# Kernel optimization log

Measured on AMD Instinct MI355X. Metric: run time of the kernel, lower is better.

## Reference

```python
import jax, jax.numpy as jnp
import numpy as np

B, T, H, N = 1, 256, 32, 128
HN = H * N
KVH = 8
KV_DIM = KVH * N
KV_REPEAT = HN // KV_DIM
ROPE_THETA = 10000.0
EPS = 1e-6
NTK_ALPHA = 10.0
YARN_MAX = 4096.0
LORA_W, LORA_A, LORA_V, LORA_G = 64, 64, 32, 128
LAYER_ID = 1


def t5_rmsnorm(x, w):
    xf = x.astype(jnp.float32)
    var = jnp.mean(xf * xf, axis=-1, keepdims=True)
    return (w * (xf * jax.lax.rsqrt(var + EPS))).astype(x.dtype)


def rotate_half(x):
    h = x.shape[-1] // 2
    return jnp.concatenate([-x[..., h:], x[..., :h]], axis=-1)


def rope_cache(cache_pos, seq_len, rotary_dim):
    # YaRN-style mix of short/long inv_freq, per compute_rope_cache_range
    half = rotary_dim // 2
    fs = jnp.arange(half, dtype=jnp.float32)
    inv_short = 1.0 / ROPE_THETA ** (fs / half)
    inv_long = 1.0 / (ROPE_THETA * NTK_ALPHA ** (fs / half))
    pos = cache_pos.astype(jnp.float32) + jnp.arange(seq_len, dtype=jnp.float32)[None, :]  # [B,T]
    mix = jnp.clip(pos / YARN_MAX, 0.0, 1.0)[..., None]
    freqs = (1.0 - mix) * (pos[..., None] * inv_short) + mix * (pos[..., None] * inv_long)
    emb = jnp.concatenate([freqs, freqs], axis=-1)  # [B,T,rotary_dim]
    return jnp.cos(emb), jnp.sin(emb)


def _forward(x_in, v_first, state, cache_position, w0, w1, w2, a0, a1, a2, v0, v1, v2, g1, g2,
             r_k, R_, K_, V_, O_, R_bias, K_bias, V_bias, ln_r, ln_k, ln1, ln2):
    x = t5_rmsnorm(x_in, ln1)  # [B,T,HN]
    # float path of fpx_matmul: x @ W.T (+ bias), i.e. the dequantized math
    r = x @ R_.T + R_bias
    k = x @ K_.T + K_bias
    v = x @ V_.T + V_bias
    r = t5_rmsnorm(r.reshape(B, T, H, N), ln_r)      # [B,T,H,N]
    k = t5_rmsnorm(k.reshape(B, T, KVH, N), ln_k)    # [B,T,KVH,N]
    cos, sin = rope_cache(cache_position, T, N)      # [B,T,N]
    cos_, sin_ = cos[:, :, None, :], sin[:, :, None, :]
    r = r * cos_ + rotate_half(r) * sin_
    k = k * cos_ + rotate_half(k) * sin_
    # decay lora: w = -softplus(-(tanh(x@w1)@w2 + w0)) - 0.5
    w = jnp.tanh(x @ w1) @ w2 + w0
    w = -jax.nn.softplus(-w) - 0.5
    # GQA repeat_kv: each kv head repeated KV_REPEAT times contiguously
    v = v.reshape(B, T, KVH, N)
    k = jnp.repeat(k, KV_REPEAT, axis=2).reshape(B, T, HN)
    v = jnp.repeat(v, KV_REPEAT, axis=2).reshape(B, T, HN)
    a = jax.nn.sigmoid((x @ a1) @ a2 + a0)
    g = jax.nn.sigmoid(x @ g1) @ g2
    k4 = k.reshape(B, T, H, N)
    kk = (k4 / jnp.maximum(jnp.linalg.norm(k4, axis=-1, keepdims=True), 1e-12)).reshape(B, T, HN)
    k = k * (1.0 - w + a)
    aa = -kk
    bb = kk * a
    if LAYER_ID == 0:
        v_first = v
    else:
        gate = jax.nn.sigmoid((x @ v1) @ v2 + v0)
        v = v + (v_first - v) * gate
    w = -jnp.exp(w.astype(jnp.float32))  # log-decay for the recurrence

    def to_tm(t):  # [B,T,HN] or [B,T,H,N] -> time-major [T,B,H,N]
        return jnp.moveaxis(t.reshape(B, T, H, N), 1, 0)

    rt, wt, kt, vt, at, bt = map(to_tm, (r, w, k, v, aa, bb))

    def step(S, inp):
        # RWKV-7: S = S*diag(exp(w)) + S @ (a b^T) + v k^T ; out = S @ r
        r_t, w_t, k_t, v_t, a_t, b_t = inp
        sa = jnp.einsum('bhij,bhj->bhi', S, a_t)
        S = S * jnp.exp(w_t)[:, :, None, :] + sa[..., None] * b_t[:, :, None, :] + v_t[..., None] * k_t[:, :, None, :]
        return S, jnp.einsum('bhij,bhj->bhi', S, r_t)

    S_final, outs = jax.lax.scan(step, state.astype(jnp.float32), (rt, wt, kt, vt, at, bt))
    xx = jnp.moveaxis(outs, 0, 1).reshape(B, T, HN) * (float(N) ** -0.5)
    bonus = jnp.sum(r.reshape(B, T, H, N) * k.reshape(B, T, H, N) * r_k, axis=-1, keepdims=True) * v.reshape(B, T, H, N)
    xx = xx.astype(r.dtype) + bonus.reshape(B, T, HN)
    x_res = x_in + (xx * g) @ O_.T
    out = t5_rmsnorm(x_res, ln2)
    return out, x[:, -1], S_final, v_first, x_res


def setup_inputs() -> dict:
    key = jax.random.key(0)
    ks = iter(jax.random.split(key, 32))
    rn = lambda *s: jax.random.normal(next(ks), s, dtype=jnp.float32)
    wt = lambda *s: rn(*s) * 0.02
    return dict(
        x_in=rn(B, T, HN),
        v_first=rn(B, T, HN),
        state=jnp.zeros((B, H, N, N), jnp.float32),
        cache_position=jnp.zeros((B, 1), jnp.int32),
        w0=wt(HN), w1=wt(HN, LORA_W), w2=wt(LORA_W, HN),
        a0=wt(HN), a1=wt(HN, LORA_A), a2=wt(LORA_A, HN),
        v0=wt(HN), v1=wt(HN, LORA_V), v2=wt(LORA_V, HN),
        g1=wt(HN, LORA_G), g2=wt(LORA_G, HN),
        r_k=wt(H, N),
        R_=wt(HN, HN), K_=wt(KV_DIM, HN), V_=wt(KV_DIM, HN), O_=wt(HN, HN),
        R_bias=wt(HN), K_bias=wt(KV_DIM), V_bias=wt(KV_DIM),
        ln_r=jnp.ones((N,), jnp.float32), ln_k=jnp.ones((N,), jnp.float32),
        ln1=jnp.ones((HN,), jnp.float32), ln2=jnp.ones((HN,), jnp.float32),
    )


def reference(x_in, v_first, state, cache_position, w0, w1, w2, a0, a1, a2, v0, v1, v2, g1, g2,
              r_k, R_, K_, V_, O_, R_bias, K_bias, V_bias, ln_r, ln_k, ln1, ln2):
    return _forward(x_in, v_first, state, cache_position, w0, w1, w2, a0, a1, a2, v0, v1, v2,
                    g1, g2, r_k, R_, K_, V_, O_, R_bias, K_bias, V_bias, ln_r, ln_k, ln1, ln2)
```

## Files before the change

### kernel.cpp

```cpp
#include <hip/hip_runtime.h>
#include <cstdint>
#include <cstddef>

#define T_ 256
#define HN_ 4096
#define H_ 32
#define N_ 128
#define SR_ 6464

typedef __attribute__((ext_vector_type(8))) short short8;
typedef __attribute__((ext_vector_type(4))) float f32x4;

__device__ __forceinline__ short f2bf(float f) {
    uint32_t u = __builtin_bit_cast(uint32_t, f);
    u = (u + 0x7fffu + ((u >> 16) & 1u)) >> 16;
    return (short)u;
}
__device__ __forceinline__ short f2bfc(float f) {
    return (short)((__builtin_bit_cast(uint32_t, f) + 0x8000u) >> 16);
}
__device__ __forceinline__ short8 cvt8r(float4 lo, float4 hi) {
    short8 v;
    v[0] = f2bfc(lo.x); v[1] = f2bfc(lo.y); v[2] = f2bfc(lo.z); v[3] = f2bfc(lo.w);
    v[4] = f2bfc(hi.x); v[5] = f2bfc(hi.y); v[6] = f2bfc(hi.z); v[7] = f2bfc(hi.w);
    return v;
}
__device__ __forceinline__ f32x4 mfma16(short8 a, short8 b, f32x4 c) {
    return __builtin_amdgcn_mfma_f32_16x16x32_bf16(a, b, c, 0, 0, 0);
}
__device__ __forceinline__ float sigm(float x) { return 1.f / (1.f + expf(-x)); }
__device__ __forceinline__ float splus(float x) { return (x > 20.f) ? x : log1pf(expf(x)); }

__device__ __forceinline__ float bf1(ushort u) {
    return __builtin_bit_cast(float, (uint32_t)u << 16);
}
__device__ __forceinline__ void bf4(float* d, const ushort* p) {
    uint2 u = *(const uint2*)p;
    d[0] = __builtin_bit_cast(float, u.x << 16);
    d[1] = __builtin_bit_cast(float, u.x & 0xffff0000u);
    d[2] = __builtin_bit_cast(float, u.y << 16);
    d[3] = __builtin_bit_cast(float, u.y & 0xffff0000u);
}
__device__ __forceinline__ void gload_lds16(const void* g, void* l) {
    __builtin_amdgcn_global_load_lds(
        (const __attribute__((address_space(1))) void*)g,
        (__attribute__((address_space(3))) void*)l, 16, 0, 0);
}

template <int CTRL>
__device__ __forceinline__ float dpp_add(float v) {
    int p = __builtin_amdgcn_mov_dpp(__builtin_bit_cast(int, v), CTRL, 0xF, 0xF, true);
    return v + __builtin_bit_cast(float, p);
}
__device__ __forceinline__ float reduce32(float v) {
    v = dpp_add<0xB1>(v);
    v = dpp_add<0x4E>(v);
    v = dpp_add<0x124>(v);
    v = dpp_add<0x128>(v);
    v += __shfl_xor(v, 16);
    return v;
}

__device__ __forceinline__ void gemm_core(
    const ushort* __restrict__ A, const float* __restrict__ Brow,
    int kbeg, float* LB, f32x4 acc[2][2]) {
    const int tid = threadIdx.x, wid = tid >> 6, l = tid & 63;
    const int ar = l & 15, ak = (l >> 4) * 8;
    const int mBase = wid * 32;

    const int p1 = tid, p2 = tid + 512;
    const int r1 = p1 >> 5, c1 = (p1 & 31) ^ (r1 & 7);
    const int r2 = p2 >> 5, c2 = (p2 & 31) ^ (r2 & 7);
    const float* sb1 = Brow + (size_t)r1 * 4096 + kbeg + c1 * 4;
    const float* sb2 = Brow + (size_t)r2 * 4096 + kbeg + c2 * 4;
    float* d1 = LB + wid * 256;
    float* d2 = LB + 2048 + wid * 256;

    const ushort* pa0 = A + (size_t)(mBase + ar) * 4096 + kbeg + ak;
    const ushort* pa1 = pa0 + (size_t)16 * 4096;

    const int rb0 = ar * 128, rb1 = (16 + ar) * 128;
    const int sx = ar & 7;
    const int cb = (l >> 4) * 2;

    short8 Ae[8], Ao[8];

#define STAGEB(s, rb) { \
    gload_lds16(sb1 + (size_t)(s) * 128, d1 + (rb) * 4096); \
    gload_lds16(sb2 + (size_t)(s) * 128, d2 + (rb) * 4096); }

#define LA(B_, s) { \
    B_[0] = *(const short8*)(pa0 + (size_t)(s) * 128);      \
    B_[1] = *(const short8*)(pa1 + (size_t)(s) * 128);      \
    B_[2] = *(const short8*)(pa0 + (size_t)(s) * 128 + 32); \
    B_[3] = *(const short8*)(pa1 + (size_t)(s) * 128 + 32); \
    B_[4] = *(const short8*)(pa0 + (size_t)(s) * 128 + 64); \
    B_[5] = *(const short8*)(pa1 + (size_t)(s) * 128 + 64); \
    B_[6] = *(const short8*)(pa0 + (size_t)(s) * 128 + 96); \
    B_[7] = *(const short8*)(pa1 + (size_t)(s) * 128 + 96); }

#define CKK(kk, B_, Lb_) { \
    const int cc = (kk) * 8 + cb; \
    float4 l0 = *(const float4*)(Lb_ + rb0 + ((cc ^ sx) * 4)); \
    float4 h0 = *(const float4*)(Lb_ + rb0 + (((cc + 1) ^ sx) * 4)); \
    float4 l1 = *(const float4*)(Lb_ + rb1 + ((cc ^ sx) * 4)); \
    float4 h1 = *(const float4*)(Lb_ + rb1 + (((cc + 1) ^ sx) * 4)); \
    short8 b0 = cvt8r(l0, h0), b1 = cvt8r(l1, h1); \
    acc[0][0] = mfma16(B_[2 * (kk)], b0, acc[0][0]); \
    acc[0][1] = mfma16(B_[2 * (kk)], b1, acc[0][1]); \
    acc[1][0] = mfma16(B_[2 * (kk) + 1], b0, acc[1][0]); \
    acc[1][1] = mfma16(B_[2 * (kk) + 1], b1, acc[1][1]); }

#define COMPUTE(rb, B_) { const float* Lb_ = LB + (rb) * 4096; \
    CKK(0, B_, Lb_) CKK(1, B_, Lb_) CKK(2, B_, Lb_) CKK(3, B_, Lb_) }

    STAGEB(0, 0)
    LA(Ae, 0)
    STAGEB(1, 1)

    for (int su = 0; su < 4; su++) {
        const int s0 = su * 2, s1 = su * 2 + 1;
        LA(Ao, (s0 + 1 < 8) ? s0 + 1 : 7)
        STAGEB((s0 + 2 < 8) ? s0 + 2 : 7, (s0 + 2) % 3)
        asm volatile("s_waitcnt vmcnt(12)" ::: "memory");
        __builtin_amdgcn_s_barrier();
        __builtin_amdgcn_sched_barrier(0);
        COMPUTE(s0 % 3, Ae)
        __builtin_amdgcn_s_barrier();

        LA(Ae, (s1 + 1 < 8) ? s1 + 1 : 7)
        STAGEB((s1 + 2 < 8) ? s1 + 2 : 7, (s1 + 2) % 3)
        asm volatile("s_waitcnt vmcnt(12)" ::: "memory");
        __builtin_amdgcn_s_barrier();
        __builtin_amdgcn_sched_barrier(0);
        COMPUTE(s1 % 3, Ao)
        __builtin_amdgcn_s_barrier();
    }
    asm volatile("s_waitcnt vmcnt(0)" ::: "memory");
#undef STAGEB
#undef LA
#undef CKK
#undef COMPUTE
}

__global__ __launch_bounds__(256) void rmsnorm_k(const float* __restrict__ in,
                                                 const float* __restrict__ w,
                                                 float* __restrict__ outF,
                                                 ushort* __restrict__ outB,
                                                 float* __restrict__ lastrow) {
    int t = blockIdx.x, tid = threadIdx.x;
    const float4* in4 = (const float4*)(in + (size_t)t * HN_);
    const float4* w4 = (const float4*)w;
    float4 v[4]; float ss = 0.f;
#pragma unroll
    for (int q = 0; q < 4; q++) {
        v[q] = in4[q * 256 + tid];
        ss += v[q].x * v[q].x + v[q].y * v[q].y + v[q].z * v[q].z + v[q].w * v[q].w;
    }
#pragma unroll
    for (int o = 32; o; o >>= 1) ss += __shfl_down(ss, o);
    __shared__ float red[4];
    if ((tid & 63) == 0) red[tid >> 6] = ss;
    __syncthreads();
    float tot = red[0] + red[1] + red[2] + red[3];
    float sc = rsqrtf(tot * (1.f / HN_) + 1e-6f);
#pragma unroll
    for (int q = 0; q < 4; q++) {
        float4 wv = w4[q * 256 + tid];
        float4 r;
        r.x = wv.x * v[q].x * sc; r.y = wv.y * v[q].y * sc;
        r.z = wv.z * v[q].z * sc; r.w = wv.w * v[q].w * sc;
        int idx = q * 256 + tid;
        if (outF) ((float4*)(outF + (size_t)t * HN_))[idx] = r;
        if (outB) {
            ushort4 b;
            b.x = (ushort)f2bf(r.x); b.y = (ushort)f2bf(r.y);
            b.z = (ushort)f2bf(r.z); b.w = (ushort)f2bf(r.w);
            ((ushort4*)(outB + (size_t)t * HN_))[idx] = b;
        }
        if (lastrow && t == T_ - 1) ((float4*)lastrow)[idx] = r;
    }
}

__global__ __launch_bounds__(512, 2) void gemm_rkvt(
    const ushort* __restrict__ A,
    const float* __restrict__ Rw, const float* __restrict__ Kw,
    const float* __restrict__ Vw, const float* __restrict__ WT,
    float* __restrict__ COMB) {
    __shared__ __align__(16) float LB[12288];
    const int tid = threadIdx.x, wid = tid >> 6, l = tid & 63;
    const int mBase = wid * 32;
    const int nB = blockIdx.x * 32;
    const int kbeg = blockIdx.y * 1024;

    const float* Bp; int brow;
    if (nB < 4096)      { Bp = Rw; brow = nB; }
    else if (nB < 5120) { Bp = Kw; brow = nB - 4096; }
    else if (nB < 6144) { Bp = Vw; brow = nB - 5120; }
    else                { Bp = WT; brow = nB - 6144; }

    f32x4 acc[2][2];
#pragma unroll
    for (int i = 0; i < 2; i++)
#pragma unroll
        for (int j = 0; j < 2; j++) acc[i][j] = f32x4{0.f, 0.f, 0.f, 0.f};

    gemm_core(A, Bp + (size_t)brow * 4096, kbeg, LB, acc);

    const int rl = (l >> 4) * 4, cl = l & 15;
#pragma unroll
    for (int mf = 0; mf < 2; mf++)
#pragma unroll
        for (int nf = 0; nf < 2; nf++)
#pragma unroll
            for (int e = 0; e < 4; e++)
                unsafeAtomicAdd(&COMB[(size_t)(mBase + mf * 16 + rl + e) * SR_ + nB + nf * 16 + cl],
                                acc[mf][nf][e]);
}

__global__ __launch_bounds__(512, 2) void gemm_o(
    const ushort* __restrict__ A,
    const float* __restrict__ B,
    float* __restrict__ C) {
    __shared__ __align__(16) float LB[12288];
    const int tid = threadIdx.x, wid = tid >> 6, l = tid & 63;
    const int mBase = wid * 32;
    const int nB = blockIdx.x * 32;
    const int kbeg = blockIdx.y * 1024;

    f32x4 acc[2][2];
#pragma unroll
    for (int i = 0; i < 2; i++)
#pragma unroll
        for (int j = 0; j < 2; j++) acc[i][j] = f32x4{0.f, 0.f, 0.f, 0.f};

    gemm_core(A, B + (size_t)nB * 4096, kbeg, LB, acc);

    const int rl = (l >> 4) * 4, cl = l & 15;
#pragma unroll
    for (int mf = 0; mf < 2; mf++)
#pragma unroll
        for (int nf = 0; nf < 2; nf++)
#pragma unroll
            for (int e = 0; e < 4; e++)
                unsafeAtomicAdd(&C[(size_t)(mBase + mf * 16 + rl + e) * 4096 + nB + nf * 16 + cl],
                                acc[mf][nf][e]);
}

__global__ __launch_bounds__(512) void gemm_s2(
    const ushort* __restrict__ TCB,
    const float* __restrict__ w2, const float* __restrict__ a2,
    const float* __restrict__ v2, const float* __restrict__ g2,
    const float* __restrict__ w0, const float* __restrict__ a0,
    const float* __restrict__ v0,
    float* __restrict__ WPRE, float* __restrict__ APRE,
    float* __restrict__ VGPRE, float* __restrict__ GARR) {
    const int z = blockIdx.y;
    int Aoff, K; const float* B; const float* bias; float* out;
    if (z == 0)      { Aoff = 0;   K = 64;  B = w2; bias = w0;      out = WPRE; }
    else if (z == 1) { Aoff = 64;  K = 64;  B = a2; bias = a0;      out = APRE; }
    else if (z == 2) { Aoff = 128; K = 32;  B = v2; bias = v0;      out = VGPRE; }
    else             { Aoff = 160; K = 128; B = g2; bias = nullptr; out = GARR; }

    const int tid = threadIdx.x, wid = tid >> 6, l = tid & 63;
    const int ar = l & 15, ak = (l >> 4) * 8;
    const int mBase = wid * 32;
    const int nB = blockIdx.x * 32;

    f32x4 acc[2][2];
#pragma unroll
    for (int i = 0; i < 2; i++)
#pragma unroll
        for (int j = 0; j < 2; j++) acc[i][j] = f32x4{0.f, 0.f, 0.f, 0.f};

    for (int k0 = 0; k0 < K; k0 += 32) {
        const ushort* pA = TCB + (size_t)(mBase + ar) * 320 + Aoff + k0 + ak;
        short8 av0 = *(const short8*)pA;
        short8 av1 = *(const short8*)(pA + (size_t)16 * 320);
        short8 bv0, bv1;
#pragma unroll
        for (int e = 0; e < 8; e++) {
            bv0[e] = f2bfc(B[(size_t)(k0 + ak + e) * 4096 + nB + ar]);
            bv1[e] = f2bfc(B[(size_t)(k0 + ak + e) * 4096 + nB + 16 + ar]);
        }
        acc[0][0] = mfma16(av0, bv0, acc[0][0]);
        acc[0][1] = mfma16(av0, bv1, acc[0][1]);
        acc[1][0] = mfma16(av1, bv0, acc[1][0]);
        acc[1][1] = mfma16(av1, bv1, acc[1][1]);
    }
    const int rl = (l >> 4) * 4, cl = l & 15;
#pragma unroll
    for (int mf = 0; mf < 2; mf++)
#pragma unroll
        for (int nf = 0; nf < 2; nf++) {
            int col = nB + nf * 16 + cl;
            float bv = bias ? bias[col] : 0.f;
#pragma unroll
            for (int e = 0; e < 4; e++)
                out[(size_t)(mBase + mf * 16 + rl + e) * 4096 + col] = acc[mf][nf][e] + bv;
        }
}

__global__ __launch_bounds__(256) void wcat2_k(const float* __restrict__ w1p,
                                               const float* __restrict__ a1p,
                                               const float* __restrict__ v1p,
                                               const float* __restrict__ g1p,
                                               float* __restrict__ WT) {
    const int kb = blockIdx.x * 64, tile = blockIdx.y;
    const float* src; int ldw, jo, nb, W;
    if (tile == 0)      { src = w1p; ldw = 64;  jo = 0;  nb = 0;   W = 64; }
    else if (tile == 1) { src = a1p; ldw = 64;  jo = 0;  nb = 64;  W = 64; }
    else if (tile == 2) { src = v1p; ldw = 32;  jo = 0;  nb = 128; W = 32; }
    else if (tile == 3) { src = g1p; ldw = 128; jo = 0;  nb = 160; W = 64; }
    else                { src = g1p; ldw = 128; jo = 64; nb = 224; W = 64; }
    __shared__ float lds[64][65];
    const int ti = threadIdx.x & 63, wi = threadIdx.x >> 6;
    if (ti < W)
        for (int i = wi; i < 64; i += 4)
            lds[i][ti] = src[(size_t)(kb + i) * ldw + jo + ti];
    __syncthreads();
    for (int i2 = wi; i2 < W; i2 += 4)
        WT[(size_t)(nb + i2) * 4096 + kb + ti] = lds[ti][i2];
}

__global__ __launch_bounds__(256) void init_comb_k(const float* __restrict__ Rb,
                                                   const float* __restrict__ Kb,
                                                   const float* __restrict__ Vb,
                                                   float* __restrict__ COMB) {
    int t = blockIdx.x;
    for (int c = threadIdx.x; c < SR_; c += 256) {
        float b = (c < 4096) ? Rb[c] : (c < 5120) ? Kb[c - 4096]
                : (c < 6144) ? Vb[c - 5120] : 0.f;
        COMB[(size_t)t * SR_ + c] = b;
    }
}

__global__ __launch_bounds__(256) void act_k(const float* __restrict__ COMB,
                                             ushort* __restrict__ TCB) {
    int idx = blockIdx.x * 256 + threadIdx.x;
    if (idx >= 256 * 288) return;
    int t = idx / 288, c = idx % 288;
    float v = COMB[(size_t)t * SR_ + 6144 + c];
    if (c < 64) v = tanhf(v);
    else if (c >= 160) v = sigm(v);
    TCB[t * 320 + c] = (ushort)f2bf(v);
}

__global__ void rope_k(const int* __restrict__ cpos, float* __restrict__ cosT,
                       float* __restrict__ sinT) {
    int idx = blockIdx.x * 256 + threadIdx.x;
    int t = idx >> 6, f = idx & 63;
    float pos = (float)cpos[0] + (float)t;
    float mix = fminf(fmaxf(pos * (1.f / 4096.f), 0.f), 1.f);
    float e = (float)f * (1.f / 64.f);
    float inv_s = exp2f(-13.287712379549449f * e);
    float inv_l = exp2f(-13.287712379549449f - 3.321928094887362f * e);
    float fr = pos * ((1.f - mix) * inv_s + mix * inv_l);
    cosT[idx] = cosf(fr);
    sinT[idx] = sinf(fr);
}

__global__ __launch_bounds__(256) void prep_k(
    const float* __restrict__ COMB, const float* __restrict__ wpre,
    const float* __restrict__ apre, const float* __restrict__ vgpre,
    const float* __restrict__ vfirst, const float* __restrict__ garr,
    const float* __restrict__ cosT, const float* __restrict__ sinT,
    const float* __restrict__ lnr, const float* __restrict__ lnk,
    ushort* __restrict__ SFB) {
    int t = blockIdx.x, tid = threadIdx.x;
    int w = tid >> 6, lane = tid & 63;
    float c = cosT[t * 64 + lane], s = sinT[t * 64 + lane];
    float lr0 = lnr[lane], lr1 = lnr[lane + 64];
    float lk0 = lnk[lane], lk1 = lnk[lane + 64];
    const float* r_raw = COMB;
    const float* k_raw = COMB + 4096;
    const float* v_raw = COMB + 5120;
    for (int hb = 0; hb < 8; hb++) {
        int h = hb * 4 + w;
        int kv = h >> 2;
        float r0 = r_raw[(size_t)t * SR_ + h * 128 + lane];
        float r1 = r_raw[(size_t)t * SR_ + h * 128 + 64 + lane];
        float ssum = r0 * r0 + r1 * r1;
#pragma unroll
        for (int o = 32; o; o >>= 1) ssum += __shfl_xor(ssum, o);
        float sc = rsqrtf(ssum * (1.f / 128.f) + 1e-6f);
        float rn0 = lr0 * r0 * sc, rn1 = lr1 * r1 * sc;
        float rr0 = rn0 * c - rn1 * s;
        float rr1 = rn1 * c + rn0 * s;
        float k0 = k_raw[(size_t)t * SR_ + kv * 128 + lane];
        float k1 = k_raw[(size_t)t * SR_ + kv * 128 + 64 + lane];
        float ks = k0 * k0 + k1 * k1;
#pragma unroll
        for (int o = 32; o; o >>= 1) ks += __shfl_xor(ks, o);
        float ksc = rsqrtf(ks * (1.f / 128.f) + 1e-6f);
        float kn0 = lk0 * k0 * ksc, kn1 = lk1 * k1 * ksc;
        float kr0 = kn0 * c - kn1 * s;
        float kr1 = kn1 * c + kn0 * s;
        float nr = kr0 * kr0 + kr1 * kr1;
#pragma unroll
        for (int o = 32; o; o >>= 1) nr += __shfl_xor(nr, o);
        float inv = 1.f / fmaxf(sqrtf(nr), 1e-12f);
        float kk0 = kr0 * inv, kk1 = kr1 * inv;
        int c0 = h * 128 + lane, c1 = c0 + 64;
        size_t tb = (size_t)t * HN_;

        float wv0 = -splus(-wpre[tb + c0]) - 0.5f;
        float wv1 = -splus(-wpre[tb + c1]) - 0.5f;
        float dec0 = expf(-expf(wv0));
        float dec1 = expf(-expf(wv1));
        float av0 = sigm(apre[tb + c0]);
        float av1 = sigm(apre[tb + c1]);
        float vg0 = sigm(vgpre[tb + c0]);
        float vg1 = sigm(vgpre[tb + c1]);
        float vraw0 = v_raw[(size_t)t * SR_ + kv * 128 + lane];
        float vraw1 = v_raw[(size_t)t * SR_ + kv * 128 + 64 + lane];
        float vf0 = vraw0 + (vfirst[tb + c0] - vraw0) * vg0;
        float vf1 = vraw1 + (vfirst[tb + c1] - vraw1) * vg1;

        ushort* sb = SFB + ((size_t)h * T_ + t) * 1024;
        sb[lane]         = (ushort)f2bf(rr0);
        sb[64 + lane]    = (ushort)f2bf(rr1);
        sb[128 + lane]   = (ushort)f2bf(kr0 * (1.f - wv0 + av0));
        sb[192 + lane]   = (ushort)f2bf(kr1 * (1.f - wv1 + av1));
        sb[256 + lane]   = (ushort)f2bf(vf0);
        sb[320 + lane]   = (ushort)f2bf(vf1);
        sb[384 + lane]   = (ushort)f2bf(-kk0);
        sb[448 + lane]   = (ushort)f2bf(-kk1);
        sb[512 + lane]   = (ushort)f2bf(kk0 * av0);
        sb[576 + lane]   = (ushort)f2bf(kk1 * av1);
        sb[640 + lane]   = (ushort)f2bf(garr[tb + c0]);
        sb[704 + lane]   = (ushort)f2bf(garr[tb + c1]);
        float* sw = (float*)(sb + 768);
        sw[lane]      = dec0;
        sw[64 + lane] = dec1;
    }
}

#define SD_ 8
#define SNB_ 9
__global__ __launch_bounds__(512) void scan_k(
    const float* __restrict__ state_in,
    const ushort* __restrict__ SFB,
    const float* __restrict__ rk,
    ushort* __restrict__ yb, float* __restrict__ Sout) {
    const int h = blockIdx.x, sp = blockIdx.y;
    const int tid = threadIdx.x;
    const int il = tid >> 5, jq = tid & 31;
    const int i = sp * 16 + il, j0 = jq * 4;
    const int wv = tid >> 6;

    float S[4];
    {
        float4 s4 = *(const float4*)(state_in + ((size_t)h * 128 + i) * 128 + j0);
        S[0] = s4.x; S[1] = s4.y; S[2] = s4.z; S[3] = s4.w;
    }
    float4 rk4 = *(const float4*)(rk + h * 128 + j0);

    __shared__ __align__(16) ushort lds_s[SNB_][1024];
    __shared__ float ybuf[2][16];
    const ushort* hbase = SFB + (size_t)h * T_ * 1024;

    auto STAGE = [&](int buf, int t) {
        if (tid < 128) {
            const ushort* src = hbase + (size_t)(t & (T_ - 1)) * 1024 + tid * 8;
            gload_lds16(src, &lds_s[buf][wv * 512]);
        }
    };

#pragma unroll
    for (int d = 0; d < SD_; d++) STAGE(d, d);

    float cpPend = 0.f;
    int bc = 0, bs = SD_;
    for (int t = 0; t < T_; t++) {
        if (wv < 2) asm volatile("s_waitcnt vmcnt(7)" ::: "memory");
        __builtin_amdgcn_s_barrier();
        __builtin_amdgcn_sched_barrier(0);
        asm volatile("" ::: "memory");

        STAGE(bs, t + SD_);

        if (wv == 7 && (tid & 63) < 16 && t > 1) {
            int ln = tid & 63;
            yb[(size_t)(t - 2) * HN_ + h * 128 + sp * 16 + ln] =
                (ushort)f2bf(ybuf[t & 1][ln]);
        }

        if (t > 0) {
            float cr = reduce32(cpPend);
            if (jq == 0) ybuf[(t - 1) & 1][il] = cr;
        }

        const ushort* L = lds_s[bc];
        float r_[4], k_[4], a_[4], b_[4];
        bf4(r_, L + j0);
        bf4(k_, L + 128 + j0);
        bf4(a_, L + 384 + j0);
        bf4(b_, L + 512 + j0);
        float vi = bf1(L[256 + i]);
        float gv = bf1(L[640 + i]);
        const float* Ld = (const float*)(L + 768);
        float4 w4 = *(const float4*)&Ld[j0];

        float sa = fmaf(S[0], a_[0], fmaf(S[1], a_[1], fmaf(S[2], a_[2], S[3] * a_[3])));
        sa = reduce32(sa);

        S[0] = fmaf(vi, k_[0], fmaf(sa, b_[0], S[0] * w4.x));
        S[1] = fmaf(vi, k_[1], fmaf(sa, b_[1], S[1] * w4.y));
        S[2] = fmaf(vi, k_[2], fmaf(sa, b_[2], S[2] * w4.z));
        S[3] = fmaf(vi, k_[3], fmaf(sa, b_[3], S[3] * w4.w));

        float od = fmaf(S[0], r_[0], fmaf(S[1], r_[1], fmaf(S[2], r_[2], S[3] * r_[3])));
        float bd = fmaf(r_[0] * k_[0], rk4.x, fmaf(r_[1] * k_[1], rk4.y,
                   fmaf(r_[2] * k_[2], rk4.z, r_[3] * k_[3] * rk4.w)));
        cpPend = fmaf(od, 0.08838834764831845f, bd * vi) * gv;

        bc = (bc + 1 == SNB_) ? 0 : bc + 1;
        bs = (bs + 1 == SNB_) ? 0 : bs + 1;
    }

    __builtin_amdgcn_s_barrier();
    {
        float cr = reduce32(cpPend);
        if (jq == 0)
            yb[(size_t)(T_ - 1) * HN_ + h * 128 + i] = (ushort)f2bf(cr);
    }
    if (wv == 7 && (tid & 63) < 16) {
        int ln = tid & 63;
        yb[(size_t)(T_ - 2) * HN_ + h * 128 + sp * 16 + ln] =
            (ushort)f2bf(ybuf[(T_ - 2) & 1][ln]);
    }

    float* p = Sout + ((size_t)h * 128 + i) * 128 + j0;
    *(float4*)p = make_float4(S[0], S[1], S[2], S[3]);
}

extern "C" void kernel_launch(void* const* d_in, const int* in_sizes, int n_in,
                              void* d_out, int out_size, void* d_ws, size_t ws_size,
                              hipStream_t stream) {
    const float* x_in   = (const float*)d_in[0];
    const float* vfirst = (const float*)d_in[1];
    const float* state  = (const float*)d_in[2];
    const int*   cpos   = (const int*)d_in[3];
    const float* w0 = (const float*)d_in[4];
    const float* w1 = (const float*)d_in[5];
    const float* w2 = (const float*)d_in[6];
    const float* a0 = (const float*)d_in[7];
    const float* a1 = (const float*)d_in[8];
    const float* a2 = (const float*)d_in[9];
    const float* v0 = (const float*)d_in[10];
    const float* v1 = (const float*)d_in[11];
    const float* v2 = (const float*)d_in[12];
    const float* g1 = (const float*)d_in[13];
    const float* g2 = (const float*)d_in[14];
    const float* r_k = (const float*)d_in[15];
    const float* R_ = (const float*)d_in[16];
    const float* K_ = (const float*)d_in[17];
    const float* V_ = (const float*)d_in[18];
    const float* O_ = (const float*)d_in[19];
    const float* Rb = (const float*)d_in[20];
    const float* Kb = (const float*)d_in[21];
    const float* Vb = (const float*)d_in[22];
    const float* ln_r = (const float*)d_in[23];
    const float* ln_k = (const float*)d_in[24];
    const float* ln1 = (const float*)d_in[25];
    const float* ln2 = (const float*)d_in[26];

    float* ws = (float*)d_ws;
    constexpr size_t OFF_XB   = 0;
    constexpr size_t OFF_COMB = 524288;
    constexpr size_t OFF_WT   = 2179072;
    constexpr size_t OFF_TCB  = 3489792;
    constexpr size_t OFF_WPRE = 3530752;
    constexpr size_t OFF_APRE = 4579328;
    constexpr size_t OFF_VGPRE= 5627904;
    constexpr size_t OFF_G    = 6676480;
    constexpr size_t OFF_COS  = 7725056;
    constexpr size_t OFF_SIN  = 7741440;
    constexpr size_t OFF_SF   = 7757824;
    constexpr size_t OFF_YB   = OFF_XB;

    ushort* XB  = (ushort*)(ws + OFF_XB);
    float* COMB = ws + OFF_COMB;
    float* WT   = ws + OFF_WT;
    ushort* TCB = (ushort*)(ws + OFF_TCB);
    float* WPRE = ws + OFF_WPRE;
    float* APRE = ws + OFF_APRE;
    float* VGPRE= ws + OFF_VGPRE;
    float* GARR = ws + OFF_G;
    float* COST = ws + OFF_COS;
    float* SINT = ws + OFF_SIN;
    ushort* SFB = (ushort*)(ws + OFF_SF);
    ushort* YB  = (ushort*)(ws + OFF_YB);

    float* out = (float*)d_out;
    float* out0  = out;
    float* xlast = out + 1048576;
    float* Sfin  = out + 1052672;
    float* vfout = out + 1576960;
    float* xres  = out + 2625536;

    hipMemcpyAsync(vfout, vfirst, (size_t)1048576 * 4, hipMemcpyDeviceToDevice, stream);
    hipMemcpyAsync(xres, x_in, (size_t)1048576 * 4, hipMemcpyDeviceToDevice, stream);

    rmsnorm_k<<<T_, 256, 0, stream>>>(x_in, ln1, nullptr, XB, xlast);

    wcat2_k<<<dim3(64, 5), 256, 0, stream>>>(w1, a1, v1, g1, WT);
    hipMemsetAsync(WT + (size_t)288 * 4096, 0, (size_t)32 * 4096 * 4, stream);
    init_comb_k<<<T_, 256, 0, stream>>>(Rb, Kb, Vb, COMB);

    gemm_rkvt<<<dim3(202, 4), 512, 0, stream>>>(XB, R_, K_, V_, WT, COMB);

    act_k<<<288, 256, 0, stream>>>(COMB, TCB);

    gemm_s2<<<dim3(128, 4), 512, 0, stream>>>(TCB, w2, a2, v2, g2, w0, a0, v0,
                                              WPRE, APRE, VGPRE, GARR);

    rope_k<<<64, 256, 0, stream>>>(cpos, COST, SINT);

    prep_k<<<T_, 256, 0, stream>>>(COMB, WPRE, APRE, VGPRE, vfirst, GARR,
                                   COST, SINT, ln_r, ln_k, SFB);

    scan_k<<<dim3(32, 8), 512, 0, stream>>>(state, SFB, r_k, YB, Sfin);

    gemm_o<<<dim3(128, 4), 512, 0, stream>>>(YB, O_, xres);

    rmsnorm_k<<<T_, 256, 0, stream>>>(xres, ln2, out0, nullptr, nullptr);
}
```

Baseline: 329.3 us.

## Process two heads per scan block to interleave independent recurrences

```diff
diff --git a/kernel.cpp b/kernel.cpp
--- a/kernel.cpp
+++ b/kernel.cpp
@@ -443,26 +443,34 @@
     const ushort* __restrict__ SFB,
     const float* __restrict__ rk,
     ushort* __restrict__ yb, float* __restrict__ Sout) {
-    const int h = blockIdx.x, sp = blockIdx.y;
+    const int hp = blockIdx.x, sp = blockIdx.y;
+    const int h0 = hp * 2, h1 = hp * 2 + 1;
     const int tid = threadIdx.x;
     const int il = tid >> 5, jq = tid & 31;
     const int i = sp * 16 + il, j0 = jq * 4;
     const int wv = tid >> 6;
 
-    float S[4];
+    float SA[4], SB[4];
     {
-        float4 s4 = *(const float4*)(state_in + ((size_t)h * 128 + i) * 128 + j0);
-        S[0] = s4.x; S[1] = s4.y; S[2] = s4.z; S[3] = s4.w;
-    }
-    float4 rk4 = *(const float4*)(rk + h * 128 + j0);
-
-    __shared__ __align__(16) ushort lds_s[SNB_][1024];
-    __shared__ float ybuf[2][16];
-    const ushort* hbase = SFB + (size_t)h * T_ * 1024;
+        float4 s4 = *(const float4*)(state_in + ((size_t)h0 * 128 + i) * 128 + j0);
+        SA[0] = s4.x; SA[1] = s4.y; SA[2] = s4.z; SA[3] = s4.w;
+        float4 s5 = *(const float4*)(state_in + ((size_t)h1 * 128 + i) * 128 + j0);
+        SB[0] = s5.x; SB[1] = s5.y; SB[2] = s5.z; SB[3] = s5.w;
+    }
+    float4 rkA = *(const float4*)(rk + h0 * 128 + j0);
+    float4 rkB = *(const float4*)(rk + h1 * 128 + j0);
+
+    __shared__ __align__(16) ushort lds_s[SNB_][2048];
+    __shared__ float ybuf[2][32];
+    const ushort* hb0 = SFB + (size_t)h0 * T_ * 1024;
+    const ushort* hb1 = SFB + (size_t)h1 * T_ * 1024;
 
     auto STAGE = [&](int buf, int t) {
-        if (tid < 128) {
-            const ushort* src = hbase + (size_t)(t & (T_ - 1)) * 1024 + tid * 8;
+        if (tid < 256) {
+            int tw = t & (T_ - 1);
+            const ushort* src = (tid < 128)
+                ? hb0 + (size_t)tw * 1024 + tid * 8
+                : hb1 + (size_t)tw * 1024 + (tid - 128) * 8;
             gload_lds16(src, &lds_s[buf][wv * 512]);
         }
     };
@@ -470,50 +478,67 @@
 #pragma unroll
     for (int d = 0; d < SD_; d++) STAGE(d, d);
 
-    float cpPend = 0.f;
+    float cpA = 0.f, cpB = 0.f;
     int bc = 0, bs = SD_;
     for (int t = 0; t < T_; t++) {
-        if (wv < 2) asm volatile("s_waitcnt vmcnt(7)" ::: "memory");
+        if (wv < 4) asm volatile("s_waitcnt vmcnt(7)" ::: "memory");
         __builtin_amdgcn_s_barrier();
         __builtin_amdgcn_sched_barrier(0);
         asm volatile("" ::: "memory");
 
         STAGE(bs, t + SD_);
 
-        if (wv == 7 && (tid & 63) < 16 && t > 1) {
+        if (wv == 7 && (tid & 63) < 32 && t > 1) {
             int ln = tid & 63;
-            yb[(size_t)(t - 2) * HN_ + h * 128 + sp * 16 + ln] =
+            int hh = (ln < 16) ? h0 : h1;
+            yb[(size_t)(t - 2) * HN_ + hh * 128 + sp * 16 + (ln & 15)] =
                 (ushort)f2bf(ybuf[t & 1][ln]);
         }
 
         if (t > 0) {
-            float cr = reduce32(cpPend);
-            if (jq == 0) ybuf[(t - 1) & 1][il] = cr;
+            float crA = reduce32(cpA);
+            float crB = reduce32(cpB);
+            if (jq == 0) {
+                ybuf[(t - 1) & 1][il] = crA;
+                ybuf[(t - 1) & 1][16 + il] = crB;
+            }
         }
 
-        const ushort* L = lds_s[bc];
-        float r_[4], k_[4], a_[4], b_[4];
-        bf4(r_, L + j0);
-        bf4(k_, L + 128 + j0);
-        bf4(a_, L + 384 + j0);
-        bf4(b_, L + 512 + j0);
-        float vi = bf1(L[256 + i]);
-        float gv = bf1(L[640 + i]);
-        const float* Ld = (const float*)(L + 768);
-        float4 w4 = *(const float4*)&Ld[j0];
-
-        float sa = fmaf(S[0], a_[0], fmaf(S[1], a_[1], fmaf(S[2], a_[2], S[3] * a_[3])));
-        sa = reduce32(sa);
-
-        S[0] = fmaf(vi, k_[0], fmaf(sa, b_[0], S[0] * w4.x));
-        S[1] = fmaf(vi, k_[1], fmaf(sa, b_[1], S[1] * w4.y));
-        S[2] = fmaf(vi, k_[2], fmaf(sa, b_[2], S[2] * w4.z));
-        S[3] = fmaf(vi, k_[3], fmaf(sa, b_[3], S[3] * w4.w));
-
-        float od = fmaf(S[0], r_[0], fmaf(S[1], r_[1], fmaf(S[2], r_[2], S[3] * r_[3])));
-        float bd = fmaf(r_[0] * k_[0], rk4.x, fmaf(r_[1] * k_[1], rk4.y,
-                   fmaf(r_[2] * k_[2], rk4.z, r_[3] * k_[3] * rk4.w)));
-        cpPend = fmaf(od, 0.08838834764831845f, bd * vi) * gv;
+        const ushort* L0 = &lds_s[bc][0];
+        const ushort* L1 = &lds_s[bc][1024];
+        float rA[4], kA[4], aA[4], bA[4];
+        float rB[4], kB[4], aB[4], bB[4];
+        bf4(rA, L0 + j0);        bf4(rB, L1 + j0);
+        bf4(kA, L0 + 128 + j0);  bf4(kB, L1 + 128 + j0);
+        bf4(aA, L0 + 384 + j0);  bf4(aB, L1 + 384 + j0);
+        bf4(bA, L0 + 512 + j0);  bf4(bB, L1 + 512 + j0);
+        float viA = bf1(L0[256 + i]), viB = bf1(L1[256 + i]);
+        float gvA = bf1(L0[640 + i]), gvB = bf1(L1[640 + i]);
+        float4 wA = *(const float4*)((const float*)(L0 + 768) + j0);
+        float4 wB = *(const float4*)((const float*)(L1 + 768) + j0);
+
+        float saA = fmaf(SA[0], aA[0], fmaf(SA[1], aA[1], fmaf(SA[2], aA[2], SA[3] * aA[3])));
+        float saB = fmaf(SB[0], aB[0], fmaf(SB[1], aB[1], fmaf(SB[2], aB[2], SB[3] * aB[3])));
+        saA = reduce32(saA);
+        saB = reduce32(saB);
+
+        SA[0] = fmaf(viA, kA[0], fmaf(saA, bA[0], SA[0] * wA.x));
+        SB[0] = fmaf(viB, kB[0], fmaf(saB, bB[0], SB[0] * wB.x));
+        SA[1] = fmaf(viA, kA[1], fmaf(saA, bA[1], SA[1] * wA.y));
+        SB[1] = fmaf(viB, kB[1], fmaf(saB, bB[1], SB[1] * wB.y));
+        SA[2] = fmaf(viA, kA[2], fmaf(saA, bA[2], SA[2] * wA.z));
+        SB[2] = fmaf(viB, kB[2], fmaf(saB, bB[2], SB[2] * wB.z));
+        SA[3] = fmaf(viA, kA[3], fmaf(saA, bA[3], SA[3] * wA.w));
+        SB[3] = fmaf(viB, kB[3], fmaf(saB, bB[3], SB[3] * wB.w));
+
+        float odA = fmaf(SA[0], rA[0], fmaf(SA[1], rA[1], fmaf(SA[2], rA[2], SA[3] * rA[3])));
+        float odB = fmaf(SB[0], rB[0], fmaf(SB[1], rB[1], fmaf(SB[2], rB[2], SB[3] * rB[3])));
+        float bdA = fmaf(rA[0] * kA[0], rkA.x, fmaf(rA[1] * kA[1], rkA.y,
+                    fmaf(rA[2] * kA[2], rkA.z, rA[3] * kA[3] * rkA.w)));
+        float bdB = fmaf(rB[0] * kB[0], rkB.x, fmaf(rB[1] * kB[1], rkB.y,
+                    fmaf(rB[2] * kB[2], rkB.z, rB[3] * kB[3] * rkB.w)));
+        cpA = fmaf(odA, 0.08838834764831845f, bdA * viA) * gvA;
+        cpB = fmaf(odB, 0.08838834764831845f, bdB * viB) * gvB;
 
         bc = (bc + 1 == SNB_) ? 0 : bc + 1;
         bs = (bs + 1 == SNB_) ? 0 : bs + 1;
@@ -521,18 +546,24 @@
 
     __builtin_amdgcn_s_barrier();
     {
-        float cr = reduce32(cpPend);
-        if (jq == 0)
-            yb[(size_t)(T_ - 1) * HN_ + h * 128 + i] = (ushort)f2bf(cr);
-    }
-    if (wv == 7 && (tid & 63) < 16) {
+        float crA = reduce32(cpA);
+        float crB = reduce32(cpB);
+        if (jq == 0) {
+            yb[(size_t)(T_ - 1) * HN_ + h0 * 128 + i] = (ushort)f2bf(crA);
+            yb[(size_t)(T_ - 1) * HN_ + h1 * 128 + i] = (ushort)f2bf(crB);
+        }
+    }
+    if (wv == 7 && (tid & 63) < 32) {
         int ln = tid & 63;
-        yb[(size_t)(T_ - 2) * HN_ + h * 128 + sp * 16 + ln] =
+        int hh = (ln < 16) ? h0 : h1;
+        yb[(size_t)(T_ - 2) * HN_ + hh * 128 + sp * 16 + (ln & 15)] =
             (ushort)f2bf(ybuf[(T_ - 2) & 1][ln]);
     }
 
-    float* p = Sout + ((size_t)h * 128 + i) * 128 + j0;
-    *(float4*)p = make_float4(S[0], S[1], S[2], S[3]);
+    float* pA = Sout + ((size_t)h0 * 128 + i) * 128 + j0;
+    *(float4*)pA = make_float4(SA[0], SA[1], SA[2], SA[3]);
+    float* pB = Sout + ((size_t)h1 * 128 + i) * 128 + j0;
+    *(float4*)pB = make_float4(SB[0], SB[1], SB[2], SB[3]);
 }
 
 extern "C" void kernel_launch(void* const* d_in, const int* in_sizes, int n_in,
@@ -621,7 +652,7 @@
     prep_k<<<T_, 256, 0, stream>>>(COMB, WPRE, APRE, VGPRE, vfirst, GARR,
                                    COST, SINT, ln_r, ln_k, SFB);
 
-    scan_k<<<dim3(32, 8), 512, 0, stream>>>(state, SFB, r_k, YB, Sfin);
+    scan_k<<<dim3(16, 8), 512, 0, stream>>>(state, SFB, r_k, YB, Sfin);
 
     gemm_o<<<dim3(128, 4), 512, 0, stream>>>(YB, O_, xres);
 
```

New measurement: 395.9 us. +20.2%, slower.

## Split scan state rows across twice as many blocks with 2 columns per lane

Applied to the files above, without the earlier changes.

```diff
diff --git a/kernel.cpp b/kernel.cpp
--- a/kernel.cpp
+++ b/kernel.cpp
@@ -34,13 +34,6 @@
 __device__ __forceinline__ float bf1(ushort u) {
     return __builtin_bit_cast(float, (uint32_t)u << 16);
 }
-__device__ __forceinline__ void bf4(float* d, const ushort* p) {
-    uint2 u = *(const uint2*)p;
-    d[0] = __builtin_bit_cast(float, u.x << 16);
-    d[1] = __builtin_bit_cast(float, u.x & 0xffff0000u);
-    d[2] = __builtin_bit_cast(float, u.y << 16);
-    d[3] = __builtin_bit_cast(float, u.y & 0xffff0000u);
-}
 __device__ __forceinline__ void gload_lds16(const void* g, void* l) {
     __builtin_amdgcn_global_load_lds(
         (const __attribute__((address_space(1))) void*)g,
@@ -52,13 +45,15 @@
     int p = __builtin_amdgcn_mov_dpp(__builtin_bit_cast(int, v), CTRL, 0xF, 0xF, true);
     return v + __builtin_bit_cast(float, p);
 }
-__device__ __forceinline__ float reduce32(float v) {
+__device__ __forceinline__ float reduce64(float v) {
     v = dpp_add<0xB1>(v);
     v = dpp_add<0x4E>(v);
     v = dpp_add<0x124>(v);
     v = dpp_add<0x128>(v);
-    v += __shfl_xor(v, 16);
-    return v;
+    v = dpp_add<0x142>(v);
+    v = dpp_add<0x143>(v);
+    int r = __builtin_amdgcn_readlane(__builtin_bit_cast(int, v), 63);
+    return __builtin_bit_cast(float, r);
 }
 
 __device__ __forceinline__ void gemm_core(
@@ -445,19 +440,19 @@
     ushort* __restrict__ yb, float* __restrict__ Sout) {
     const int h = blockIdx.x, sp = blockIdx.y;
     const int tid = threadIdx.x;
-    const int il = tid >> 5, jq = tid & 31;
-    const int i = sp * 16 + il, j0 = jq * 4;
-    const int wv = tid >> 6;
-
-    float S[4];
+    const int wv = tid >> 6, ln = tid & 63;
+    const int i = sp * 8 + wv;
+    const int j0 = ln * 2;
+
+    float S0, S1;
     {
-        float4 s4 = *(const float4*)(state_in + ((size_t)h * 128 + i) * 128 + j0);
-        S[0] = s4.x; S[1] = s4.y; S[2] = s4.z; S[3] = s4.w;
-    }
-    float4 rk4 = *(const float4*)(rk + h * 128 + j0);
+        float2 s2 = *(const float2*)(state_in + ((size_t)h * 128 + i) * 128 + j0);
+        S0 = s2.x; S1 = s2.y;
+    }
+    float2 rk2 = *(const float2*)(rk + h * 128 + j0);
 
     __shared__ __align__(16) ushort lds_s[SNB_][1024];
-    __shared__ float ybuf[2][16];
+    __shared__ float ybuf[2][8];
     const ushort* hbase = SFB + (size_t)h * T_ * 1024;
 
     auto STAGE = [&](int buf, int t) {
@@ -480,39 +475,37 @@
 
         STAGE(bs, t + SD_);
 
-        if (wv == 7 && (tid & 63) < 16 && t > 1) {
-            int ln = tid & 63;
-            yb[(size_t)(t - 2) * HN_ + h * 128 + sp * 16 + ln] =
+        if (wv == 7 && ln < 8 && t > 1) {
+            yb[(size_t)(t - 2) * HN_ + h * 128 + sp * 8 + ln] =
                 (ushort)f2bf(ybuf[t & 1][ln]);
         }
 
         if (t > 0) {
-            float cr = reduce32(cpPend);
-            if (jq == 0) ybuf[(t - 1) & 1][il] = cr;
+            float cr = reduce64(cpPend);
+            if (ln == 0) ybuf[(t - 1) & 1][wv] = cr;
         }
 
         const ushort* L = lds_s[bc];
-        float r_[4], k_[4], a_[4], b_[4];
-        bf4(r_, L + j0);
-        bf4(k_, L + 128 + j0);
-        bf4(a_, L + 384 + j0);
-        bf4(b_, L + 512 + j0);
+        uint ur = *(const uint*)(L + j0);
+        uint uk = *(const uint*)(L + 128 + j0);
+        uint ua = *(const uint*)(L + 384 + j0);
+        uint ub = *(const uint*)(L + 512 + j0);
+        float r0 = bf1((ushort)ur), r1 = bf1((ushort)(ur >> 16));
+        float k0 = bf1((ushort)uk), k1 = bf1((ushort)(uk >> 16));
+        float a0 = bf1((ushort)ua), a1 = bf1((ushort)(ua >> 16));
+        float b0 = bf1((ushort)ub), b1 = bf1((ushort)(ub >> 16));
         float vi = bf1(L[256 + i]);
         float gv = bf1(L[640 + i]);
-        const float* Ld = (const float*)(L + 768);
-        float4 w4 = *(const float4*)&Ld[j0];
-
-        float sa = fmaf(S[0], a_[0], fmaf(S[1], a_[1], fmaf(S[2], a_[2], S[3] * a_[3])));
-        sa = reduce32(sa);
-
-        S[0] = fmaf(vi, k_[0], fmaf(sa, b_[0], S[0] * w4.x));
-        S[1] = fmaf(vi, k_[1], fmaf(sa, b_[1], S[1] * w4.y));
-        S[2] = fmaf(vi, k_[2], fmaf(sa, b_[2], S[2] * w4.z));
-        S[3] = fmaf(vi, k_[3], fmaf(sa, b_[3], S[3] * w4.w));
-
-        float od = fmaf(S[0], r_[0], fmaf(S[1], r_[1], fmaf(S[2], r_[2], S[3] * r_[3])));
-        float bd = fmaf(r_[0] * k_[0], rk4.x, fmaf(r_[1] * k_[1], rk4.y,
-                   fmaf(r_[2] * k_[2], rk4.z, r_[3] * k_[3] * rk4.w)));
+        float2 w2 = *(const float2*)((const float*)(L + 768) + j0);
+
+        float sa = fmaf(S0, a0, S1 * a1);
+        sa = reduce64(sa);
+
+        S0 = fmaf(vi, k0, fmaf(sa, b0, S0 * w2.x));
+        S1 = fmaf(vi, k1, fmaf(sa, b1, S1 * w2.y));
+
+        float od = fmaf(S0, r0, S1 * r1);
+        float bd = fmaf(r0 * k0, rk2.x, r1 * k1 * rk2.y);
         cpPend = fmaf(od, 0.08838834764831845f, bd * vi) * gv;
 
         bc = (bc + 1 == SNB_) ? 0 : bc + 1;
@@ -521,18 +514,17 @@
 
     __builtin_amdgcn_s_barrier();
     {
-        float cr = reduce32(cpPend);
-        if (jq == 0)
+        float cr = reduce64(cpPend);
+        if (ln == 0)
             yb[(size_t)(T_ - 1) * HN_ + h * 128 + i] = (ushort)f2bf(cr);
     }
-    if (wv == 7 && (tid & 63) < 16) {
-        int ln = tid & 63;
-        yb[(size_t)(T_ - 2) * HN_ + h * 128 + sp * 16 + ln] =
+    if (wv == 7 && ln < 8) {
+        yb[(size_t)(T_ - 2) * HN_ + h * 128 + sp * 8 + ln] =
             (ushort)f2bf(ybuf[(T_ - 2) & 1][ln]);
     }
 
     float* p = Sout + ((size_t)h * 128 + i) * 128 + j0;
-    *(float4*)p = make_float4(S[0], S[1], S[2], S[3]);
+    *(float2*)p = make_float2(S0, S1);
 }
 
 extern "C" void kernel_launch(void* const* d_in, const int* in_sizes, int n_in,
@@ -621,7 +613,7 @@
     prep_k<<<T_, 256, 0, stream>>>(COMB, WPRE, APRE, VGPRE, vfirst, GARR,
                                    COST, SINT, ln_r, ln_k, SFB);
 
-    scan_k<<<dim3(32, 8), 512, 0, stream>>>(state, SFB, r_k, YB, Sfin);
+    scan_k<<<dim3(32, 16), 512, 0, stream>>>(state, SFB, r_k, YB, Sfin);
 
     gemm_o<<<dim3(128, 4), 512, 0, stream>>>(YB, O_, xres);
 
```

Result: no change. 324.2 us (-1.5%).
